# Performance work log

Measured on AMD Instinct MI355X. Metric: run time of the kernel, lower is better.

The kernel has to match this reference:

```python
import jax, jax.numpy as jnp
import numpy as np

V = 59      # input features (mimic_59f)
H = 128     # hidden size
B = 2048
T = 96

def _uniform(key, shape, fan_in):
    s = 1.0 / np.sqrt(fan_in)
    return jax.random.uniform(key, shape, jnp.float32, -s, s)

def setup_inputs() -> dict:
    key = jax.random.key(0)
    ks = jax.random.split(key, 20)
    x = jax.random.normal(ks[0], (B, T, V), jnp.float32)
    mask = (jax.random.uniform(ks[1], (B, T, V)) < 0.8).astype(jnp.float32)
    deltas = jax.random.uniform(ks[2], (B, T, V), jnp.float32)
    return {
        'x': x, 'mask': mask, 'deltas': deltas,
        # temp_decay_h: Decay(V -> H)
        'Wdh': _uniform(ks[3], (H, V), V), 'bdh': _uniform(ks[4], (H,), V),
        # temp_decay_x: Decay(V -> V, diag)
        'Wdx': _uniform(ks[5], (V, V), V), 'bdx': _uniform(ks[6], (V,), V),
        # hist: Linear(H -> V)
        'Wh': _uniform(ks[7], (V, H), H), 'bh': _uniform(ks[8], (V,), H),
        'Wf': _uniform(ks[9], (V, V), V), 'bf': _uniform(ks[10], (V,), V),
        # weight_combine: Linear(2V -> V)
        'Wc': _uniform(ks[11], (V, 2 * V), 2 * V), 'bc': _uniform(ks[12], (V,), 2 * V),
        # GRUCell(2V -> H): gates ordered [r, z, n]
        'Wih': _uniform(ks[13], (3 * H, 2 * V), 2 * V), 'Whh': _uniform(ks[14], (3 * H, H), H),
        'bih': _uniform(ks[15], (3 * H,), H), 'bhh': _uniform(ks[16], (3 * H,), H),
    }


def reference(x, mask, deltas, Wdh, bdh, Wdx, bdx, Wh, bh, Wf, bf, Wc, bc, Wih, Whh, bih, bhh):
    Bb, Tt, Vv = x.shape
    eye = jnp.eye(Vv, dtype=x.dtype)
    Wdx_d = Wdx * eye            # diagonal decay
    Wf_m = Wf * (1.0 - eye)

    def step(h, inp):
        x_t, m_t, d_t = inp                                  # each [B, V]
        gamma_h = jnp.exp(-jax.nn.relu(d_t @ Wdh.T + bdh))   # [B, H]
        h = h * gamma_h
        x_h = h @ Wh.T + bh                                   # [B, V]
        x_r = m_t * x_t + (1.0 - m_t) * x_h
        xu = x_r @ Wf_m.T + bf
        gamma_x = jnp.exp(-jax.nn.relu(d_t @ Wdx_d.T + bdx))
        beta = jnp.concatenate([gamma_x, m_t], axis=1) @ Wc.T + bc
        x_comb = beta * xu + (1.0 - beta) * x_h
        loss_t = jnp.sum(jnp.abs(x_t - x_comb) * m_t) / (jnp.sum(m_t) + 1e-5)
        x_imp_t = m_t * x_t + (1.0 - m_t) * x_comb
        inp_t = jnp.concatenate([x_imp_t, m_t], axis=1)       # [B, 2V]
        gi = inp_t @ Wih.T + bih                              # [B, 3H]
        gh = h @ Whh.T + bhh
        ir, iz, inn = jnp.split(gi, 3, axis=1)
        hr, hz, hn = jnp.split(gh, 3, axis=1)
        r = jax.nn.sigmoid(ir + hr)
        z = jax.nn.sigmoid(iz + hz)
        n = jnp.tanh(inn + r * hn)
        h_new = (1.0 - z) * n + z * h
        return h_new, (x_imp_t, h_new, loss_t)

    xs = (jnp.swapaxes(x, 0, 1), jnp.swapaxes(mask, 0, 1), jnp.swapaxes(deltas, 0, 1))
    h0 = jnp.zeros((Bb, Wdh.shape[0]), x.dtype)
    _, (x_imp, Hiddens, losses) = jax.lax.scan(step, h0, xs)
    return (jnp.swapaxes(x_imp, 0, 1),      # imputation [B, T, V]
            jnp.sum(losses),                 # xloss scalar
            jnp.swapaxes(Hiddens, 0, 1))     # hidden_state [B, T, H]
```

## Files before the change

### kernel.cpp

```cpp
#include <hip/hip_runtime.h>
#include <hip/hip_bf16.h>
#include <math.h>

#define VF 59
#define HF 128
#define BB 2048
#define TT 96
#define MR 16
#define NBLK (BB / MR)
#define NTH 512

typedef __attribute__((ext_vector_type(8))) short short8;
typedef __attribute__((ext_vector_type(4))) float f32x4;

#define MFMA(a, b, c) __builtin_amdgcn_mfma_f32_16x16x32_bf16((a), (b), (c), 0, 0, 0)

#define WF_INV   0
#define WF_ACC   96
#define WF_DWDX  192
#define WF_END   256
#define U_B1  (WF_END * 2)
#define U_B2  (U_B1 + 8192)
#define U_B3  (U_B2 + 8192)
#define U_B4  (U_B3 + 4096)
#define U_B5  (U_B4 + 8192)
#define U_B6  (U_B5 + 49152)

#define LOSS_IDX (BB * TT * VF)
#define OFF_HID  (BB * TT * VF + 1)

#define S_AD    0
#define S_AH    1152
#define S_AXR   3328
#define S_AGM   4480
#define S_AIM0  6656
#define S_AIM1  8832
#define F_SX    5504
#define F_SM    6464
#define F_SB    7424
#define F_RED   8448
#define F_IDT   8456
#define F_TOT   8552

__device__ __forceinline__ ushort f2bf(float f) {
    __hip_bfloat16 h = __float2bfloat16(f);
    return *reinterpret_cast<ushort*>(&h);
}
__device__ __forceinline__ float sigm(float v) { return 1.f / (1.f + __expf(-v)); }
__device__ __forceinline__ float tanh_f(float v) {
    float c = fminf(fmaxf(v, -15.f), 15.f);
    float e = __expf(-2.f * c);
    return (1.f - e) / (1.f + e);
}

__device__ __forceinline__ void block_sync() {
    asm volatile("s_waitcnt lgkmcnt(0)" ::: "memory");
    __builtin_amdgcn_s_barrier();
    asm volatile("" ::: "memory");
}

__global__ __launch_bounds__(128) void prep_zero(float* __restrict__ ws, float* __restrict__ loss_ptr) {
    int tid = threadIdx.x;
    if (tid < TT) ws[WF_ACC + tid] = 0.f;
    if (tid == 96) loss_ptr[0] = 0.f;
}

__global__ __launch_bounds__(512) void prep_acc(const float* __restrict__ mask, float* __restrict__ ws) {
    __shared__ float acc[TT];
    int tid = threadIdx.x;
    if (tid < TT) acc[tid] = 0.f;
    __syncthreads();
    int wv = tid >> 6, lane = tid & 63;
    int b = blockIdx.x * 8 + wv;
    const float* base = mask + (size_t)b * (TT * VF);
    #pragma unroll 4
    for (int t = 0; t < TT; ++t) {
        float v = (lane < VF) ? base[t * VF + lane] : 0.f;
        #pragma unroll
        for (int off = 32; off > 0; off >>= 1) v += __shfl_down(v, off);
        if (lane == 0) atomicAdd(&acc[t], v);
    }
    __syncthreads();
    if (tid < TT) atomicAdd(&ws[WF_ACC + tid], acc[tid]);
}

__device__ void packB(const float* __restrict__ W, int G, int K, int tiles, int KS,
                      int zdiag, ushort* __restrict__ dst, int gtid, int gstride) {
    int total = tiles * KS * 512;
    for (int idx = gtid; idx < total; idx += gstride) {
        int j  = idx & 7;
        int l  = (idx >> 3) & 63;
        int tk = idx >> 9;
        int ks = tk % KS;
        int tile = tk / KS;
        int g = tile * 16 + (l & 15);
        int k = ks * 32 + ((l >> 4) << 3) + j;
        float v = 0.f;
        if (g < G && k < K) v = W[g * K + k];
        if (zdiag && g == k) v = 0.f;
        dst[idx] = f2bf(v);
    }
}

__global__ __launch_bounds__(256) void prep_pack(
    const float* __restrict__ Wdh, const float* __restrict__ Wdx,
    const float* __restrict__ Wh,  const float* __restrict__ Wf,
    const float* __restrict__ Wc,  const float* __restrict__ Wih,
    const float* __restrict__ Whh, float* __restrict__ ws)
{
    int blk = blockIdx.x, tid = threadIdx.x;
    if (blk == 64) {
        if (tid < TT) ws[WF_INV + tid] = 1.f / (ws[WF_ACC + tid] + 1e-5f);
        if (tid < VF) ws[WF_DWDX + tid] = Wdx[tid * VF + tid];
        return;
    }
    ushort* wsu = (ushort*)ws;
    int gtid = blk * 256 + tid;
    int gstride = 64 * 256;
    packB(Wdh, HF,     VF,     8,  2, 0, wsu + U_B1, gtid, gstride);
    packB(Wh,  VF,     HF,     4,  4, 0, wsu + U_B2, gtid, gstride);
    packB(Wf,  VF,     VF,     4,  2, 1, wsu + U_B3, gtid, gstride);
    packB(Wc,  VF,     2*VF,   4,  4, 0, wsu + U_B4, gtid, gstride);
    packB(Wih, 3*HF,   2*VF,   24, 4, 0, wsu + U_B5, gtid, gstride);
    packB(Whh, 3*HF,   HF,     24, 4, 0, wsu + U_B6, gtid, gstride);
}

__global__ __launch_bounds__(NTH, 2) void rits_main(
    const float* __restrict__ x, const float* __restrict__ mask, const float* __restrict__ deltas,
    const float* __restrict__ bdh, const float* __restrict__ bdx, const float* __restrict__ bh,
    const float* __restrict__ bf,  const float* __restrict__ bc,
    const float* __restrict__ bih, const float* __restrict__ bhh,
    const float* __restrict__ ws, float* __restrict__ out)
{
    __shared__ __align__(16) float smf[F_TOT];
    ushort* smu = (ushort*)smf;

    const int tid  = threadIdx.x;
    const int lane = tid & 63;
    const int w    = tid >> 6;
    const int ln15 = lane & 15;
    const int quad = lane >> 4;
    const int b0   = blockIdx.x * MR;

    const ushort* wsu = (const ushort*)ws;
    const short8* B1 = (const short8*)(wsu + U_B1);
    const short8* B2 = (const short8*)(wsu + U_B2);
    const short8* B3 = (const short8*)(wsu + U_B3);
    const short8* B4 = (const short8*)(wsu + U_B4);
    const short8* B5 = (const short8*)(wsu + U_B5);
    const short8* B6 = (const short8*)(wsu + U_B6);

    short8 wB1[2];
    #pragma unroll
    for (int i = 0; i < 2; ++i) wB1[i] = B1[(w * 2 + i) * 64 + lane];
    short8 wB24[4];
    #pragma unroll
    for (int ks = 0; ks < 4; ++ks)
        wB24[ks] = (w < 4) ? B2[(w * 4 + ks) * 64 + lane]
                           : B4[((w - 4) * 4 + ks) * 64 + lane];
    short8 wB3[2];
    #pragma unroll
    for (int i = 0; i < 2; ++i) wB3[i] = B3[(((w < 4) ? w : (w - 4)) * 2 + i) * 64 + lane];
    short8 wB5[12], wB6[12];
    #pragma unroll
    for (int tt = 0; tt < 3; ++tt)
        #pragma unroll
        for (int ks = 0; ks < 4; ++ks) {
            wB5[tt * 4 + ks] = B5[((w + tt * 8) * 4 + ks) * 64 + lane];
            wB6[tt * 4 + ks] = B6[((w + tt * 8) * 4 + ks) * 64 + lane];
        }

    const int jH = w * 16 + ln15;
    const float c_bdh = bdh[jH];
    const float c_br  = bih[jH]       + bhh[jH];
    const float c_bz  = bih[jH + 128] + bhh[jH + 128];
    const float c_bin = bih[jH + 256];
    const float c_bhn = bhh[jH + 256];
    const int vC = (w < 4 ? w : w - 4) * 16 + ln15;
    const float c_bh = (vC < VF) ? bh[vC] : 0.f;
    const float c_bf = (vC < VF) ? bf[vC] : 0.f;
    const float c_bc = (vC < VF) ? bc[vC] : 0.f;

    const int q  = tid & 255;
    const int lr = q >> 4;
    const int lc = q & 15;
    const size_t rowbase = (size_t)(b0 + lr) * (TT * VF);
    const float* px = x + rowbase;
    const float* pm = mask + rowbase;
    const float* pd = deltas + rowbase;
    float wdx4[4], bdx4[4];
    #pragma unroll
    for (int k = 0; k < 4; ++k) {
        int v = lc + 16 * k;
        wdx4[k] = (v < VF) ? ws[WF_DWDX + v] : 0.f;
        bdx4[k] = (v < VF) ? bdx[v] : 0.f;
    }

    float hreg[4] = {0.f, 0.f, 0.f, 0.f};

    for (int i = tid; i < F_TOT; i += NTH) smf[i] = 0.f;
    __syncthreads();

    if (tid < TT) smf[F_IDT + tid] = ws[WF_INV + tid];
    if (w >= 4) {
        #pragma unroll
        for (int k = 0; k < 4; ++k) {
            int v = lc + 16 * k;
            if (v < VF) {
                float xv = px[v], mv = pm[v], dv = pd[v];
                smf[F_SX + lr * 60 + v] = xv;
                smf[F_SM + lr * 60 + v] = mv;
                ushort mb = f2bf(mv);
                smu[S_AGM  + lr * 136 + 59 + v] = mb;
                smu[S_AIM0 + lr * 136 + 59 + v] = mb;
                float gx = __expf(-fmaxf(fmaf(dv, wdx4[k], bdx4[k]), 0.f));
                smu[S_AGM + lr * 136 + v] = f2bf(gx);
            }
        }
    }
    __syncthreads();

    float loss_acc = 0.f;

    for (int t = 0; t < TT; ++t) {
        float pxv[4], pmv[4], pdv[4];
        if (w >= 4 && t + 1 < TT) {
            const size_t toff = (size_t)(t + 1) * VF;
            #pragma unroll
            for (int k = 0; k < 4; ++k) {
                int v = lc + 16 * k;
                if (v < VF) { pxv[k] = px[toff + v]; pmv[k] = pm[toff + v]; pdv[k] = pd[toff + v]; }
            }
        }

        short8 ah[4];
        #pragma unroll
        for (int ks = 0; ks < 4; ++ks)
            ah[ks] = *(const short8*)(smu + S_AH + ln15 * 136 + quad * 8 + ks * 32);
        f32x4 gHa[3];
        #pragma unroll
        for (int tt = 0; tt < 3; ++tt) gHa[tt] = (f32x4){0.f, 0.f, 0.f, 0.f};
        float xh[4], mmv[4];
        if (w < 4) {
            f32x4 acc = {0.f, 0.f, 0.f, 0.f};
            #pragma unroll
            for (int ks = 0; ks < 4; ++ks) acc = MFMA(ah[ks], wB24[ks], acc);
            #pragma unroll
            for (int tt = 0; tt < 3; ++tt)
                #pragma unroll
                for (int ks = 0; ks < 4; ++ks) gHa[tt] = MFMA(ah[ks], wB6[tt * 4 + ks], gHa[tt]);
            if (vC < VF) {
                #pragma unroll
                for (int i = 0; i < 4; ++i) {
                    int m = quad * 4 + i;
                    xh[i] = acc[i] + c_bh;
                    float mm = smf[F_SM + m * 60 + vC];
                    mmv[i] = mm;
                    float xr = fmaf(mm, smf[F_SX + m * 60 + vC], (1.f - mm) * xh[i]);
                    smu[S_AXR + m * 72 + vC] = f2bf(xr);
                }
            }
        } else {
            short8 ag[4];
            #pragma unroll
            for (int ks = 0; ks < 4; ++ks)
                ag[ks] = *(const short8*)(smu + S_AGM + ln15 * 136 + quad * 8 + ks * 32);
            f32x4 acc = {0.f, 0.f, 0.f, 0.f};
            #pragma unroll
            for (int ks = 0; ks < 4; ++ks) acc = MFMA(ag[ks], wB24[ks], acc);
            #pragma unroll
            for (int tt = 0; tt < 3; ++tt)
                #pragma unroll
                for (int ks = 0; ks < 4; ++ks) gHa[tt] = MFMA(ah[ks], wB6[tt * 4 + ks], gHa[tt]);
            if (vC < VF) {
                #pragma unroll
                for (int i = 0; i < 4; ++i)
                    smf[F_SB + (quad * 4 + i) * 64 + vC] = acc[i] + c_bc;
            }
        }
        block_sync();

        if (w < 4) {
            short8 a0 = *(const short8*)(smu + S_AXR + ln15 * 72 + quad * 8);
            short8 a1 = *(const short8*)(smu + S_AXR + ln15 * 72 + quad * 8 + 32);
            f32x4 acc = {0.f, 0.f, 0.f, 0.f};
            acc = MFMA(a0, wB3[0], acc);
            acc = MFMA(a1, wB3[1], acc);
            if (vC < VF) {
                const float idt = smf[F_IDT + t];
                const int aimW = S_AIM0 + (t & 1) * 2176;
                #pragma unroll
                for (int i = 0; i < 4; ++i) {
                    int m = quad * 4 + i;
                    float xu   = acc[i] + c_bf;
                    float beta = smf[F_SB + m * 64 + vC];
                    float xc   = beta * xu + (1.f - beta) * xh[i];
                    float mm   = mmv[i];
                    float xv   = smf[F_SX + m * 60 + vC];
                    loss_acc += fabsf(xv - xc) * mm * idt;
                    float xi = fmaf(mm, xv, (1.f - mm) * xc);
                    out[(size_t)(b0 + m) * (TT * VF) + (size_t)t * VF + vC] = xi;
                    smu[aimW + m * 136 + vC] = f2bf(xi);
                }
            }
        } else if (t + 1 < TT) {
            #pragma unroll
            for (int k = 0; k < 4; ++k) {
                int v = lc + 16 * k;
                if (v < VF) {
                    smu[S_AD + lr * 72 + v] = f2bf(pdv[k]);
                    float gx = __expf(-fmaxf(fmaf(pdv[k], wdx4[k], bdx4[k]), 0.f));
                    smu[S_AGM + lr * 136 + v] = f2bf(gx);
                }
            }
        }
        block_sync();

        {
            const int aimR = S_AIM0 + (t & 1) * 2176;
            short8 ai[4];
            #pragma unroll
            for (int ks = 0; ks < 4; ++ks)
                ai[ks] = *(const short8*)(smu + aimR + ln15 * 136 + quad * 8 + ks * 32);
            f32x4 gI[3];
            #pragma unroll
            for (int tt = 0; tt < 3; ++tt) gI[tt] = (f32x4){0.f, 0.f, 0.f, 0.f};
            #pragma unroll
            for (int tt = 0; tt < 3; ++tt)
                #pragma unroll
                for (int ks = 0; ks < 4; ++ks) gI[tt] = MFMA(ai[ks], wB5[tt * 4 + ks], gI[tt]);
            float gdec[4] = {0.f, 0.f, 0.f, 0.f};
            if (t + 1 < TT) {
                short8 d0 = *(const short8*)(smu + S_AD + ln15 * 72 + quad * 8);
                short8 d1 = *(const short8*)(smu + S_AD + ln15 * 72 + quad * 8 + 32);
                f32x4 gacc = {0.f, 0.f, 0.f, 0.f};
                gacc = MFMA(d0, wB1[0], gacc);
                gacc = MFMA(d1, wB1[1], gacc);
                #pragma unroll
                for (int i = 0; i < 4; ++i)
                    gdec[i] = __expf(-fmaxf(gacc[i] + c_bdh, 0.f));
            }
            #pragma unroll
            for (int i = 0; i < 4; ++i) {
                int m = quad * 4 + i;
                float r_ = sigm(gI[0][i] + gHa[0][i] + c_br);
                float z_ = sigm(gI[1][i] + gHa[1][i] + c_bz);
                float hn = gHa[2][i] + c_bhn;
                float n_ = tanh_f(fmaf(r_, hn, gI[2][i] + c_bin));
                float hnew = fmaf(z_, hreg[i] - n_, n_);
                out[OFF_HID + (size_t)(b0 + m) * (TT * HF) + (size_t)t * HF + jH] = hnew;
                float hd = hnew * gdec[i];
                hreg[i] = hd;
                if (t + 1 < TT) smu[S_AH + m * 136 + jH] = f2bf(hd);
            }
        }
        if (w >= 4 && t + 1 < TT) {
            const int aimN = S_AIM0 + ((t + 1) & 1) * 2176;
            #pragma unroll
            for (int k = 0; k < 4; ++k) {
                int v = lc + 16 * k;
                if (v < VF) {
                    smf[F_SX + lr * 60 + v] = pxv[k];
                    smf[F_SM + lr * 60 + v] = pmv[k];
                    ushort mb = f2bf(pmv[k]);
                    smu[S_AGM + lr * 136 + 59 + v] = mb;
                    smu[aimN  + lr * 136 + 59 + v] = mb;
                }
            }
        }
        block_sync();
    }

    __syncthreads();
    float vsum = loss_acc;
    for (int off = 32; off > 0; off >>= 1) vsum += __shfl_down(vsum, off);
    if (lane == 0) smf[F_RED + w] = vsum;
    __syncthreads();
    if (tid == 0) {
        float s = 0.f;
        #pragma unroll
        for (int i = 0; i < 8; ++i) s += smf[F_RED + i];
        atomicAdd(out + LOSS_IDX, s);
    }
}

extern "C" void kernel_launch(void* const* d_in, const int* in_sizes, int n_in,
                              void* d_out, int out_size, void* d_ws, size_t ws_size,
                              hipStream_t stream) {
    const float* x      = (const float*)d_in[0];
    const float* mask   = (const float*)d_in[1];
    const float* deltas = (const float*)d_in[2];
    const float* Wdh    = (const float*)d_in[3];
    const float* bdh    = (const float*)d_in[4];
    const float* Wdx    = (const float*)d_in[5];
    const float* bdx    = (const float*)d_in[6];
    const float* Wh     = (const float*)d_in[7];
    const float* bh     = (const float*)d_in[8];
    const float* Wf     = (const float*)d_in[9];
    const float* bf     = (const float*)d_in[10];
    const float* Wc     = (const float*)d_in[11];
    const float* bc     = (const float*)d_in[12];
    const float* Wih    = (const float*)d_in[13];
    const float* Whh    = (const float*)d_in[14];
    const float* bih    = (const float*)d_in[15];
    const float* bhh    = (const float*)d_in[16];
    float* out = (float*)d_out;
    float* ws  = (float*)d_ws;

    prep_zero<<<1, 128, 0, stream>>>(ws, out + LOSS_IDX);
    prep_acc<<<256, 512, 0, stream>>>(mask, ws);
    prep_pack<<<65, 256, 0, stream>>>(Wdh, Wdx, Wh, Wf, Wc, Wih, Whh, ws);
    rits_main<<<NBLK, NTH, 0, stream>>>(x, mask, deltas, bdh, bdx, bh, bf, bc,
                                        bih, bhh, ws, out);
}
```

Baseline: 533.2 us.

## Cut per-step barriers by redundantly computing x_h per wave with fragment-layout LDS

Each of waves 0-3 now computes the full x_h across all four column tiles, using the Wh weights staged in LDS, and keeps its own beta computation, where before the work was split between two wave groups. This removes one block barrier per timestep. LDS operands are stored in MFMA fragment order so each fragment is read with one vector load, gamma_x/mask buffers are double-buffered, and inputs are prefetched two steps ahead. The mask-sum prep kernel is rewritten to one row per thread. In exchange, waves 0-3 do redundant MFMA work, LDS use rises, and register pressure grows from the extra prefetch buffers.

Measured after the change: 730.7 us. 37.0% more time.

```diff
diff --git a/kernel.cpp b/kernel.cpp
--- a/kernel.cpp
+++ b/kernel.cpp
@@ -30,17 +30,18 @@
 #define OFF_HID  (BB * TT * VF + 1)
 
 #define S_AD    0
-#define S_AH    1152
-#define S_AXR   3328
-#define S_AGM   4480
-#define S_AIM0  6656
-#define S_AIM1  8832
-#define F_SX    5504
-#define F_SM    6464
-#define F_SB    7424
-#define F_RED   8448
-#define F_IDT   8456
-#define F_TOT   8552
+#define S_AH    1024
+#define S_AGM0  3072
+#define S_AGM1  5120
+#define S_AIM0  7168
+#define S_AIM1  9216
+#define S_XR    11264
+#define S_WH    15360
+#define F_SX    11776
+#define F_SM    12736
+#define F_RED   13696
+#define F_IDT   13704
+#define F_TOT   13800
 
 __device__ __forceinline__ ushort f2bf(float f) {
     __hip_bfloat16 h = __float2bfloat16(f);
@@ -52,6 +53,9 @@
     float e = __expf(-2.f * c);
     return (1.f - e) / (1.f + e);
 }
+__device__ __forceinline__ int fragIdx(int row, int col) {
+    return ((col >> 5) * 64 + ((col >> 3) & 3) * 16 + row) * 8 + (col & 7);
+}
 
 __device__ __forceinline__ void block_sync() {
     asm volatile("s_waitcnt lgkmcnt(0)" ::: "memory");
@@ -65,20 +69,19 @@
     if (tid == 96) loss_ptr[0] = 0.f;
 }
 
-__global__ __launch_bounds__(512) void prep_acc(const float* __restrict__ mask, float* __restrict__ ws) {
+__global__ __launch_bounds__(256) void prep_acc(const float* __restrict__ mask, float* __restrict__ ws) {
     __shared__ float acc[TT];
     int tid = threadIdx.x;
     if (tid < TT) acc[tid] = 0.f;
     __syncthreads();
-    int wv = tid >> 6, lane = tid & 63;
-    int b = blockIdx.x * 8 + wv;
-    const float* base = mask + (size_t)b * (TT * VF);
-    #pragma unroll 4
-    for (int t = 0; t < TT; ++t) {
-        float v = (lane < VF) ? base[t * VF + lane] : 0.f;
-        #pragma unroll
-        for (int off = 32; off > 0; off >>= 1) v += __shfl_down(v, off);
-        if (lane == 0) atomicAdd(&acc[t], v);
+    #pragma unroll
+    for (int rr = 0; rr < 2; ++rr) {
+        int row = blockIdx.x * 512 + rr * 256 + tid;
+        const float* p = mask + (size_t)row * VF;
+        float s = 0.f;
+        #pragma unroll
+        for (int v = 0; v < VF; ++v) s += p[v];
+        atomicAdd(&acc[row % TT], s);
     }
     __syncthreads();
     if (tid < TT) atomicAdd(&ws[WF_ACC + tid], acc[tid]);
@@ -144,7 +147,6 @@
 
     const ushort* wsu = (const ushort*)ws;
     const short8* B1 = (const short8*)(wsu + U_B1);
-    const short8* B2 = (const short8*)(wsu + U_B2);
     const short8* B3 = (const short8*)(wsu + U_B3);
     const short8* B4 = (const short8*)(wsu + U_B4);
     const short8* B5 = (const short8*)(wsu + U_B5);
@@ -153,14 +155,6 @@
     short8 wB1[2];
     #pragma unroll
     for (int i = 0; i < 2; ++i) wB1[i] = B1[(w * 2 + i) * 64 + lane];
-    short8 wB24[4];
-    #pragma unroll
-    for (int ks = 0; ks < 4; ++ks)
-        wB24[ks] = (w < 4) ? B2[(w * 4 + ks) * 64 + lane]
-                           : B4[((w - 4) * 4 + ks) * 64 + lane];
-    short8 wB3[2];
-    #pragma unroll
-    for (int i = 0; i < 2; ++i) wB3[i] = B3[(((w < 4) ? w : (w - 4)) * 2 + i) * 64 + lane];
     short8 wB5[12], wB6[12];
     #pragma unroll
     for (int tt = 0; tt < 3; ++tt)
@@ -169,6 +163,13 @@
             wB5[tt * 4 + ks] = B5[((w + tt * 8) * 4 + ks) * 64 + lane];
             wB6[tt * 4 + ks] = B6[((w + tt * 8) * 4 + ks) * 64 + lane];
         }
+    short8 wB3[2], wB4[4];
+    if (w < 4) {
+        #pragma unroll
+        for (int i = 0; i < 2; ++i) wB3[i] = B3[(w * 2 + i) * 64 + lane];
+        #pragma unroll
+        for (int ks = 0; ks < 4; ++ks) wB4[ks] = B4[(w * 4 + ks) * 64 + lane];
+    }
 
     const int jH = w * 16 + ln15;
     const float c_bdh = bdh[jH];
@@ -177,9 +178,14 @@
     const float c_bin = bih[jH + 256];
     const float c_bhn = bhh[jH + 256];
     const int vC = (w < 4 ? w : w - 4) * 16 + ln15;
-    const float c_bh = (vC < VF) ? bh[vC] : 0.f;
-    const float c_bf = (vC < VF) ? bf[vC] : 0.f;
-    const float c_bc = (vC < VF) ? bc[vC] : 0.f;
+    const float c_bf = (w < 4 && vC < VF) ? bf[vC] : 0.f;
+    const float c_bc = (w < 4 && vC < VF) ? bc[vC] : 0.f;
+    float c_bh4[4];
+    #pragma unroll
+    for (int tile = 0; tile < 4; ++tile) {
+        int col = tile * 16 + ln15;
+        c_bh4[tile] = (col < VF) ? bh[col] : 0.f;
+    }
 
     const int q  = tid & 255;
     const int lr = q >> 4;
@@ -201,7 +207,14 @@
     for (int i = tid; i < F_TOT; i += NTH) smf[i] = 0.f;
     __syncthreads();
 
+    {
+        const int4* src = (const int4*)(wsu + U_B2);
+        int4* dst = (int4*)(smu + S_WH);
+        for (int i = tid; i < 1024; i += NTH) dst[i] = src[i];
+    }
     if (tid < TT) smf[F_IDT + tid] = ws[WF_INV + tid];
+
+    float cxv[4], cmv[4], cdv[4];
     if (w >= 4) {
         #pragma unroll
         for (int k = 0; k < 4; ++k) {
@@ -211,10 +224,11 @@
                 smf[F_SX + lr * 60 + v] = xv;
                 smf[F_SM + lr * 60 + v] = mv;
                 ushort mb = f2bf(mv);
-                smu[S_AGM  + lr * 136 + 59 + v] = mb;
-                smu[S_AIM0 + lr * 136 + 59 + v] = mb;
+                smu[S_AGM0 + fragIdx(lr, 59 + v)] = mb;
+                smu[S_AIM0 + fragIdx(lr, 59 + v)] = mb;
                 float gx = __expf(-fmaxf(fmaf(dv, wdx4[k], bdx4[k]), 0.f));
-                smu[S_AGM + lr * 136 + v] = f2bf(gx);
+                smu[S_AGM0 + fragIdx(lr, v)] = f2bf(gx);
+                cxv[k] = px[VF + v]; cmv[k] = pm[VF + v]; cdv[k] = pd[VF + v];
             }
         }
     }
@@ -223,105 +237,108 @@
     float loss_acc = 0.f;
 
     for (int t = 0; t < TT; ++t) {
-        float pxv[4], pmv[4], pdv[4];
-        if (w >= 4 && t + 1 < TT) {
-            const size_t toff = (size_t)(t + 1) * VF;
+        const int p = t & 1;
+        const int aimC = S_AIM0 + p * 2048;
+        float nxv[4], nmv[4], ndv[4];
+        if (w >= 4 && t + 2 < TT) {
+            const size_t toff = (size_t)(t + 2) * VF;
             #pragma unroll
             for (int k = 0; k < 4; ++k) {
                 int v = lc + 16 * k;
-                if (v < VF) { pxv[k] = px[toff + v]; pmv[k] = pm[toff + v]; pdv[k] = pd[toff + v]; }
+                if (v < VF) { nxv[k] = px[toff + v]; nmv[k] = pm[toff + v]; ndv[k] = pd[toff + v]; }
             }
         }
 
         short8 ah[4];
         #pragma unroll
         for (int ks = 0; ks < 4; ++ks)
-            ah[ks] = *(const short8*)(smu + S_AH + ln15 * 136 + quad * 8 + ks * 32);
+            ah[ks] = *(const short8*)(smu + S_AH + (ks * 64 + lane) * 8);
         f32x4 gHa[3];
         #pragma unroll
         for (int tt = 0; tt < 3; ++tt) gHa[tt] = (f32x4){0.f, 0.f, 0.f, 0.f};
-        float xh[4], mmv[4];
+        #pragma unroll
+        for (int tt = 0; tt < 3; ++tt)
+            #pragma unroll
+            for (int ks = 0; ks < 4; ++ks) gHa[tt] = MFMA(ah[ks], wB6[tt * 4 + ks], gHa[tt]);
+
         if (w < 4) {
-            f32x4 acc = {0.f, 0.f, 0.f, 0.f};
-            #pragma unroll
-            for (int ks = 0; ks < 4; ++ks) acc = MFMA(ah[ks], wB24[ks], acc);
-            #pragma unroll
-            for (int tt = 0; tt < 3; ++tt)
-                #pragma unroll
-                for (int ks = 0; ks < 4; ++ks) gHa[tt] = MFMA(ah[ks], wB6[tt * 4 + ks], gHa[tt]);
+            const int agmC = S_AGM0 + p * 2048;
+            short8 ag[4];
+            #pragma unroll
+            for (int ks = 0; ks < 4; ++ks)
+                ag[ks] = *(const short8*)(smu + agmC + (ks * 64 + lane) * 8);
+            float xh_own[4], mm_own[4], xx_own[4];
+            const int xrb = S_XR + w * 1024;
+            #pragma unroll
+            for (int tile = 0; tile < 4; ++tile) {
+                short8 wh0 = *(const short8*)(smu + S_WH + ((tile * 4 + 0) * 64 + lane) * 8);
+                short8 wh1 = *(const short8*)(smu + S_WH + ((tile * 4 + 1) * 64 + lane) * 8);
+                short8 wh2 = *(const short8*)(smu + S_WH + ((tile * 4 + 2) * 64 + lane) * 8);
+                short8 wh3 = *(const short8*)(smu + S_WH + ((tile * 4 + 3) * 64 + lane) * 8);
+                f32x4 acc = {0.f, 0.f, 0.f, 0.f};
+                acc = MFMA(ah[0], wh0, acc);
+                acc = MFMA(ah[1], wh1, acc);
+                acc = MFMA(ah[2], wh2, acc);
+                acc = MFMA(ah[3], wh3, acc);
+                int col = tile * 16 + ln15;
+                if (col < VF) {
+                    #pragma unroll
+                    for (int i = 0; i < 4; ++i) {
+                        int m = quad * 4 + i;
+                        float xh = acc[i] + c_bh4[tile];
+                        float mm = smf[F_SM + m * 60 + col];
+                        float xx = smf[F_SX + m * 60 + col];
+                        float xr = fmaf(mm, xx, (1.f - mm) * xh);
+                        smu[xrb + fragIdx(m, col)] = f2bf(xr);
+                        if (tile == w) { xh_own[i] = xh; mm_own[i] = mm; xx_own[i] = xx; }
+                    }
+                }
+            }
+            asm volatile("s_waitcnt lgkmcnt(0)" ::: "memory");
+            __builtin_amdgcn_sched_barrier(0);
+            short8 xr0 = *(const short8*)(smu + xrb + (0 * 64 + lane) * 8);
+            short8 xr1 = *(const short8*)(smu + xrb + (1 * 64 + lane) * 8);
+            f32x4 xua = {0.f, 0.f, 0.f, 0.f};
+            xua = MFMA(xr0, wB3[0], xua);
+            xua = MFMA(xr1, wB3[1], xua);
+            f32x4 bacc = {0.f, 0.f, 0.f, 0.f};
+            #pragma unroll
+            for (int ks = 0; ks < 4; ++ks) bacc = MFMA(ag[ks], wB4[ks], bacc);
             if (vC < VF) {
+                const float idt = smf[F_IDT + t];
                 #pragma unroll
                 for (int i = 0; i < 4; ++i) {
                     int m = quad * 4 + i;
-                    xh[i] = acc[i] + c_bh;
-                    float mm = smf[F_SM + m * 60 + vC];
-                    mmv[i] = mm;
-                    float xr = fmaf(mm, smf[F_SX + m * 60 + vC], (1.f - mm) * xh[i]);
-                    smu[S_AXR + m * 72 + vC] = f2bf(xr);
-                }
-            }
-        } else {
-            short8 ag[4];
-            #pragma unroll
-            for (int ks = 0; ks < 4; ++ks)
-                ag[ks] = *(const short8*)(smu + S_AGM + ln15 * 136 + quad * 8 + ks * 32);
-            f32x4 acc = {0.f, 0.f, 0.f, 0.f};
-            #pragma unroll
-            for (int ks = 0; ks < 4; ++ks) acc = MFMA(ag[ks], wB24[ks], acc);
-            #pragma unroll
-            for (int tt = 0; tt < 3; ++tt)
-                #pragma unroll
-                for (int ks = 0; ks < 4; ++ks) gHa[tt] = MFMA(ah[ks], wB6[tt * 4 + ks], gHa[tt]);
-            if (vC < VF) {
-                #pragma unroll
-                for (int i = 0; i < 4; ++i)
-                    smf[F_SB + (quad * 4 + i) * 64 + vC] = acc[i] + c_bc;
-            }
-        }
-        block_sync();
-
-        if (w < 4) {
-            short8 a0 = *(const short8*)(smu + S_AXR + ln15 * 72 + quad * 8);
-            short8 a1 = *(const short8*)(smu + S_AXR + ln15 * 72 + quad * 8 + 32);
-            f32x4 acc = {0.f, 0.f, 0.f, 0.f};
-            acc = MFMA(a0, wB3[0], acc);
-            acc = MFMA(a1, wB3[1], acc);
-            if (vC < VF) {
-                const float idt = smf[F_IDT + t];
-                const int aimW = S_AIM0 + (t & 1) * 2176;
-                #pragma unroll
-                for (int i = 0; i < 4; ++i) {
-                    int m = quad * 4 + i;
-                    float xu   = acc[i] + c_bf;
-                    float beta = smf[F_SB + m * 64 + vC];
-                    float xc   = beta * xu + (1.f - beta) * xh[i];
-                    float mm   = mmv[i];
-                    float xv   = smf[F_SX + m * 60 + vC];
+                    float xu   = xua[i] + c_bf;
+                    float beta = bacc[i] + c_bc;
+                    float xc   = beta * xu + (1.f - beta) * xh_own[i];
+                    float mm   = mm_own[i];
+                    float xv   = xx_own[i];
                     loss_acc += fabsf(xv - xc) * mm * idt;
                     float xi = fmaf(mm, xv, (1.f - mm) * xc);
                     out[(size_t)(b0 + m) * (TT * VF) + (size_t)t * VF + vC] = xi;
-                    smu[aimW + m * 136 + vC] = f2bf(xi);
+                    smu[aimC + fragIdx(m, vC)] = f2bf(xi);
                 }
             }
         } else if (t + 1 < TT) {
+            const int agmN = S_AGM0 + ((t + 1) & 1) * 2048;
             #pragma unroll
             for (int k = 0; k < 4; ++k) {
                 int v = lc + 16 * k;
                 if (v < VF) {
-                    smu[S_AD + lr * 72 + v] = f2bf(pdv[k]);
-                    float gx = __expf(-fmaxf(fmaf(pdv[k], wdx4[k], bdx4[k]), 0.f));
-                    smu[S_AGM + lr * 136 + v] = f2bf(gx);
+                    smu[S_AD + fragIdx(lr, v)] = f2bf(cdv[k]);
+                    float gx = __expf(-fmaxf(fmaf(cdv[k], wdx4[k], bdx4[k]), 0.f));
+                    smu[agmN + fragIdx(lr, v)] = f2bf(gx);
                 }
             }
         }
         block_sync();
 
         {
-            const int aimR = S_AIM0 + (t & 1) * 2176;
             short8 ai[4];
             #pragma unroll
             for (int ks = 0; ks < 4; ++ks)
-                ai[ks] = *(const short8*)(smu + aimR + ln15 * 136 + quad * 8 + ks * 32);
+                ai[ks] = *(const short8*)(smu + aimC + (ks * 64 + lane) * 8);
             f32x4 gI[3];
             #pragma unroll
             for (int tt = 0; tt < 3; ++tt) gI[tt] = (f32x4){0.f, 0.f, 0.f, 0.f};
@@ -331,8 +348,8 @@
                 for (int ks = 0; ks < 4; ++ks) gI[tt] = MFMA(ai[ks], wB5[tt * 4 + ks], gI[tt]);
             float gdec[4] = {0.f, 0.f, 0.f, 0.f};
             if (t + 1 < TT) {
-                short8 d0 = *(const short8*)(smu + S_AD + ln15 * 72 + quad * 8);
-                short8 d1 = *(const short8*)(smu + S_AD + ln15 * 72 + quad * 8 + 32);
+                short8 d0 = *(const short8*)(smu + S_AD + (0 * 64 + lane) * 8);
+                short8 d1 = *(const short8*)(smu + S_AD + (1 * 64 + lane) * 8);
                 f32x4 gacc = {0.f, 0.f, 0.f, 0.f};
                 gacc = MFMA(d0, wB1[0], gacc);
                 gacc = MFMA(d1, wB1[1], gacc);
@@ -351,21 +368,26 @@
                 out[OFF_HID + (size_t)(b0 + m) * (TT * HF) + (size_t)t * HF + jH] = hnew;
                 float hd = hnew * gdec[i];
                 hreg[i] = hd;
-                if (t + 1 < TT) smu[S_AH + m * 136 + jH] = f2bf(hd);
+                if (t + 1 < TT) smu[S_AH + fragIdx(m, jH)] = f2bf(hd);
             }
         }
         if (w >= 4 && t + 1 < TT) {
-            const int aimN = S_AIM0 + ((t + 1) & 1) * 2176;
+            const int aimN = S_AIM0 + ((t + 1) & 1) * 2048;
+            const int agmN = S_AGM0 + ((t + 1) & 1) * 2048;
             #pragma unroll
             for (int k = 0; k < 4; ++k) {
                 int v = lc + 16 * k;
                 if (v < VF) {
-                    smf[F_SX + lr * 60 + v] = pxv[k];
-                    smf[F_SM + lr * 60 + v] = pmv[k];
-                    ushort mb = f2bf(pmv[k]);
-                    smu[S_AGM + lr * 136 + 59 + v] = mb;
-                    smu[aimN  + lr * 136 + 59 + v] = mb;
+                    smf[F_SX + lr * 60 + v] = cxv[k];
+                    smf[F_SM + lr * 60 + v] = cmv[k];
+                    ushort mb = f2bf(cmv[k]);
+                    smu[agmN + fragIdx(lr, 59 + v)] = mb;
+                    smu[aimN + fragIdx(lr, 59 + v)] = mb;
                 }
+            }
+            if (t + 2 < TT) {
+                #pragma unroll
+                for (int k = 0; k < 4; ++k) { cxv[k] = nxv[k]; cmv[k] = nmv[k]; cdv[k] = ndv[k]; }
             }
         }
         block_sync();
@@ -408,7 +430,7 @@
     float* ws  = (float*)d_ws;
 
     prep_zero<<<1, 128, 0, stream>>>(ws, out + LOSS_IDX);
-    prep_acc<<<256, 512, 0, stream>>>(mask, ws);
+    prep_acc<<<384, 256, 0, stream>>>(mask, ws);
     prep_pack<<<65, 256, 0, stream>>>(Wdh, Wdx, Wh, Wf, Wc, Wih, Whh, ws);
     rits_main<<<NBLK, NTH, 0, stream>>>(x, mask, deltas, bdh, bdx, bh, bf, bc,
                                         bih, bhh, ws, out);
```

## Store MFMA A-operands in fragment-native LDS layout and coalesce mask reduction

Applied to the files above, without the earlier changes.

Shared-memory activation buffers (h, gamma/mask, x_r, imputed input, deltas) are rearranged into an MFMA-fragment-ordered layout, so each lane reads its short8 operand from contiguous lane*8 addresses. This is meant to remove LDS bank conflicts on the operand loads. The beta buffer gets a per-row rotation swizzle for the same reason. Separately, the mask-sum prep kernel now stages contiguous float4 chunks into LDS and reduces whole rows per thread, replacing the per-wave shuffle reductions. The cost is scattered element stores when writing into the fragment layout.

New measurement: 527.2 us. No clear change (-1.1%).

```diff
diff --git a/kernel.cpp b/kernel.cpp
--- a/kernel.cpp
+++ b/kernel.cpp
@@ -30,17 +30,17 @@
 #define OFF_HID  (BB * TT * VF + 1)
 
 #define S_AD    0
-#define S_AH    1152
-#define S_AXR   3328
-#define S_AGM   4480
-#define S_AIM0  6656
-#define S_AIM1  8832
-#define F_SX    5504
-#define F_SM    6464
-#define F_SB    7424
-#define F_RED   8448
-#define F_IDT   8456
-#define F_TOT   8552
+#define S_AH    1024
+#define S_AGM   3072
+#define S_AIM0  5120
+#define S_AIM1  7168
+#define S_AXR   9216
+#define F_SX    5120
+#define F_SM    6080
+#define F_SB    7040
+#define F_RED   8064
+#define F_IDT   8072
+#define F_TOT   8168
 
 __device__ __forceinline__ ushort f2bf(float f) {
     __hip_bfloat16 h = __float2bfloat16(f);
@@ -52,6 +52,12 @@
     float e = __expf(-2.f * c);
     return (1.f - e) / (1.f + e);
 }
+__device__ __forceinline__ int fragIdx(int row, int col) {
+    return ((col >> 5) * 64 + ((col >> 3) & 3) * 16 + row) * 8 + (col & 7);
+}
+__device__ __forceinline__ int betaIdx(int m, int col) {
+    return m * 64 + ((col + 4 * m) & 63);
+}
 
 __device__ __forceinline__ void block_sync() {
     asm volatile("s_waitcnt lgkmcnt(0)" ::: "memory");
@@ -65,20 +71,26 @@
     if (tid == 96) loss_ptr[0] = 0.f;
 }
 
-__global__ __launch_bounds__(512) void prep_acc(const float* __restrict__ mask, float* __restrict__ ws) {
+#define PA_R 128
+__global__ __launch_bounds__(256) void prep_acc(const float* __restrict__ mask, float* __restrict__ ws) {
+    __shared__ float buf[PA_R * VF];
     __shared__ float acc[TT];
     int tid = threadIdx.x;
     if (tid < TT) acc[tid] = 0.f;
-    __syncthreads();
-    int wv = tid >> 6, lane = tid & 63;
-    int b = blockIdx.x * 8 + wv;
-    const float* base = mask + (size_t)b * (TT * VF);
-    #pragma unroll 4
-    for (int t = 0; t < TT; ++t) {
-        float v = (lane < VF) ? base[t * VF + lane] : 0.f;
-        #pragma unroll
-        for (int off = 32; off > 0; off >>= 1) v += __shfl_down(v, off);
-        if (lane == 0) atomicAdd(&acc[t], v);
+    const float4* src = (const float4*)(mask + (size_t)blockIdx.x * (PA_R * VF));
+    float4* dst = (float4*)buf;
+    #pragma unroll
+    for (int i = 0; i < 8; ++i) {
+        int idx = tid + i * 256;
+        if (idx < PA_R * VF / 4) dst[idx] = src[idx];
+    }
+    __syncthreads();
+    if (tid < PA_R) {
+        float s = 0.f;
+        #pragma unroll
+        for (int v = 0; v < VF; ++v) s += buf[tid * VF + v];
+        int t = (blockIdx.x * PA_R + tid) % TT;
+        atomicAdd(&acc[t], s);
     }
     __syncthreads();
     if (tid < TT) atomicAdd(&ws[WF_ACC + tid], acc[tid]);
@@ -211,10 +223,10 @@
                 smf[F_SX + lr * 60 + v] = xv;
                 smf[F_SM + lr * 60 + v] = mv;
                 ushort mb = f2bf(mv);
-                smu[S_AGM  + lr * 136 + 59 + v] = mb;
-                smu[S_AIM0 + lr * 136 + 59 + v] = mb;
+                smu[S_AGM  + fragIdx(lr, 59 + v)] = mb;
+                smu[S_AIM0 + fragIdx(lr, 59 + v)] = mb;
                 float gx = __expf(-fmaxf(fmaf(dv, wdx4[k], bdx4[k]), 0.f));
-                smu[S_AGM + lr * 136 + v] = f2bf(gx);
+                smu[S_AGM + fragIdx(lr, v)] = f2bf(gx);
             }
         }
     }
@@ -236,7 +248,7 @@
         short8 ah[4];
         #pragma unroll
         for (int ks = 0; ks < 4; ++ks)
-            ah[ks] = *(const short8*)(smu + S_AH + ln15 * 136 + quad * 8 + ks * 32);
+            ah[ks] = *(const short8*)(smu + S_AH + (ks * 64 + lane) * 8);
         f32x4 gHa[3];
         #pragma unroll
         for (int tt = 0; tt < 3; ++tt) gHa[tt] = (f32x4){0.f, 0.f, 0.f, 0.f};
@@ -257,14 +269,14 @@
                     float mm = smf[F_SM + m * 60 + vC];
                     mmv[i] = mm;
                     float xr = fmaf(mm, smf[F_SX + m * 60 + vC], (1.f - mm) * xh[i]);
-                    smu[S_AXR + m * 72 + vC] = f2bf(xr);
+                    smu[S_AXR + fragIdx(m, vC)] = f2bf(xr);
                 }
             }
         } else {
             short8 ag[4];
             #pragma unroll
             for (int ks = 0; ks < 4; ++ks)
-                ag[ks] = *(const short8*)(smu + S_AGM + ln15 * 136 + quad * 8 + ks * 32);
+                ag[ks] = *(const short8*)(smu + S_AGM + (ks * 64 + lane) * 8);
             f32x4 acc = {0.f, 0.f, 0.f, 0.f};
             #pragma unroll
             for (int ks = 0; ks < 4; ++ks) acc = MFMA(ag[ks], wB24[ks], acc);
@@ -274,33 +286,35 @@
                 for (int ks = 0; ks < 4; ++ks) gHa[tt] = MFMA(ah[ks], wB6[tt * 4 + ks], gHa[tt]);
             if (vC < VF) {
                 #pragma unroll
-                for (int i = 0; i < 4; ++i)
-                    smf[F_SB + (quad * 4 + i) * 64 + vC] = acc[i] + c_bc;
+                for (int i = 0; i < 4; ++i) {
+                    int m = quad * 4 + i;
+                    smf[F_SB + betaIdx(m, vC)] = acc[i] + c_bc;
+                }
             }
         }
         block_sync();
 
         if (w < 4) {
-            short8 a0 = *(const short8*)(smu + S_AXR + ln15 * 72 + quad * 8);
-            short8 a1 = *(const short8*)(smu + S_AXR + ln15 * 72 + quad * 8 + 32);
+            short8 a0 = *(const short8*)(smu + S_AXR + (0 * 64 + lane) * 8);
+            short8 a1 = *(const short8*)(smu + S_AXR + (1 * 64 + lane) * 8);
             f32x4 acc = {0.f, 0.f, 0.f, 0.f};
             acc = MFMA(a0, wB3[0], acc);
             acc = MFMA(a1, wB3[1], acc);
             if (vC < VF) {
                 const float idt = smf[F_IDT + t];
-                const int aimW = S_AIM0 + (t & 1) * 2176;
+                const int aimW = S_AIM0 + (t & 1) * 2048;
                 #pragma unroll
                 for (int i = 0; i < 4; ++i) {
                     int m = quad * 4 + i;
                     float xu   = acc[i] + c_bf;
-                    float beta = smf[F_SB + m * 64 + vC];
+                    float beta = smf[F_SB + betaIdx(m, vC)];
                     float xc   = beta * xu + (1.f - beta) * xh[i];
                     float mm   = mmv[i];
                     float xv   = smf[F_SX + m * 60 + vC];
                     loss_acc += fabsf(xv - xc) * mm * idt;
                     float xi = fmaf(mm, xv, (1.f - mm) * xc);
                     out[(size_t)(b0 + m) * (TT * VF) + (size_t)t * VF + vC] = xi;
-                    smu[aimW + m * 136 + vC] = f2bf(xi);
+                    smu[aimW + fragIdx(m, vC)] = f2bf(xi);
                 }
             }
         } else if (t + 1 < TT) {
@@ -308,20 +322,20 @@
             for (int k = 0; k < 4; ++k) {
                 int v = lc + 16 * k;
                 if (v < VF) {
-                    smu[S_AD + lr * 72 + v] = f2bf(pdv[k]);
+                    smu[S_AD + fragIdx(lr, v)] = f2bf(pdv[k]);
                     float gx = __expf(-fmaxf(fmaf(pdv[k], wdx4[k], bdx4[k]), 0.f));
-                    smu[S_AGM + lr * 136 + v] = f2bf(gx);
+                    smu[S_AGM + fragIdx(lr, v)] = f2bf(gx);
                 }
             }
         }
         block_sync();
 
         {
-            const int aimR = S_AIM0 + (t & 1) * 2176;
+            const int aimR = S_AIM0 + (t & 1) * 2048;
             short8 ai[4];
             #pragma unroll
             for (int ks = 0; ks < 4; ++ks)
-                ai[ks] = *(const short8*)(smu + aimR + ln15 * 136 + quad * 8 + ks * 32);
+                ai[ks] = *(const short8*)(smu + aimR + (ks * 64 + lane) * 8);
             f32x4 gI[3];
             #pragma unroll
             for (int tt = 0; tt < 3; ++tt) gI[tt] = (f32x4){0.f, 0.f, 0.f, 0.f};
@@ -331,8 +345,8 @@
                 for (int ks = 0; ks < 4; ++ks) gI[tt] = MFMA(ai[ks], wB5[tt * 4 + ks], gI[tt]);
             float gdec[4] = {0.f, 0.f, 0.f, 0.f};
             if (t + 1 < TT) {
-                short8 d0 = *(const short8*)(smu + S_AD + ln15 * 72 + quad * 8);
-                short8 d1 = *(const short8*)(smu + S_AD + ln15 * 72 + quad * 8 + 32);
+                short8 d0 = *(const short8*)(smu + S_AD + (0 * 64 + lane) * 8);
+                short8 d1 = *(const short8*)(smu + S_AD + (1 * 64 + lane) * 8);
                 f32x4 gacc = {0.f, 0.f, 0.f, 0.f};
                 gacc = MFMA(d0, wB1[0], gacc);
                 gacc = MFMA(d1, wB1[1], gacc);
@@ -351,11 +365,11 @@
                 out[OFF_HID + (size_t)(b0 + m) * (TT * HF) + (size_t)t * HF + jH] = hnew;
                 float hd = hnew * gdec[i];
                 hreg[i] = hd;
-                if (t + 1 < TT) smu[S_AH + m * 136 + jH] = f2bf(hd);
+                if (t + 1 < TT) smu[S_AH + fragIdx(m, jH)] = f2bf(hd);
             }
         }
         if (w >= 4 && t + 1 < TT) {
-            const int aimN = S_AIM0 + ((t + 1) & 1) * 2176;
+            const int aimN = S_AIM0 + ((t + 1) & 1) * 2048;
             #pragma unroll
             for (int k = 0; k < 4; ++k) {
                 int v = lc + 16 * k;
@@ -363,8 +377,8 @@
                     smf[F_SX + lr * 60 + v] = pxv[k];
                     smf[F_SM + lr * 60 + v] = pmv[k];
                     ushort mb = f2bf(pmv[k]);
-                    smu[S_AGM + lr * 136 + 59 + v] = mb;
-                    smu[aimN  + lr * 136 + 59 + v] = mb;
+                    smu[S_AGM + fragIdx(lr, 59 + v)] = mb;
+                    smu[aimN  + fragIdx(lr, 59 + v)] = mb;
                 }
             }
         }
@@ -408,7 +422,7 @@
     float* ws  = (float*)d_ws;
 
     prep_zero<<<1, 128, 0, stream>>>(ws, out + LOSS_IDX);
-    prep_acc<<<256, 512, 0, stream>>>(mask, ws);
+    prep_acc<<<(BB * TT) / PA_R, 256, 0, stream>>>(mask, ws);
     prep_pack<<<65, 256, 0, stream>>>(Wdh, Wdx, Wh, Wf, Wc, Wih, Whh, ws);
     rits_main<<<NBLK, NTH, 0, stream>>>(x, mask, deltas, bdh, bdx, bh, bf, bc,
                                         bih, bhh, ws, out);
```
